# Kernel tuning notes

Hardware: AMD Instinct MI355X
Metric: run time of the kernel (lower is better)

Reference implementation:

```python
import jax, jax.numpy as jnp
import numpy as np

N_NODES = 100      # fixed: actor_fc expects 6000 = 100 * 60
IN_C    = 65536    # chev_conv_state_dim
OUT_C   = 60
K       = 3        # Chebyshev order
ACTION  = 100
N_EDGES = 1600


def setup_inputs() -> dict:
    key = jax.random.key(0)
    ks = jax.random.split(key, 20)
    s = 0.02  # small init scale
    f32 = jnp.float32
    return {
        "substrate_features": jax.random.normal(ks[0], (N_NODES, IN_C), f32),
        "substrate_edge_index": jax.random.randint(ks[1], (2, N_EDGES), 0, N_NODES),
        "vnr_features": jax.random.uniform(ks[2], (1, 3), f32),
        # ChebConv params: weight [K, IN_C, OUT_C], bias [OUT_C]
        "actor_cheb_w": (jax.random.normal(ks[3], (K, IN_C, OUT_C), f32) * s),
        "actor_cheb_b": jnp.zeros((OUT_C,), f32),
        "critic_cheb_w": (jax.random.normal(ks[4], (K, IN_C, OUT_C), f32) * s),
        "critic_cheb_b": jnp.zeros((OUT_C,), f32),
        # three Linear(1,60) per head, stacked: w [3, 60], b [3, 60]
        "actor_vnr_w": jax.random.normal(ks[5], (3, OUT_C), f32) * s,
        "actor_vnr_b": jnp.zeros((3, OUT_C), f32),
        "critic_vnr_w": jax.random.normal(ks[6], (3, OUT_C), f32) * s,
        "critic_vnr_b": jnp.zeros((3, OUT_C), f32),
        # heads
        "actor_fc_w": jax.random.normal(ks[7], (N_NODES * OUT_C, ACTION), f32) * s,
        "actor_fc_b": jnp.zeros((ACTION,), f32),
        "critic_fc_w": jax.random.normal(ks[8], (N_NODES * OUT_C, 1), f32) * s,
        "critic_fc_b": jnp.zeros((1,), f32),
    }


def _cheb_conv(x, src, dst, W, b):
    """PyG ChebConv with sym normalization, lambda_max=2 => L_hat = -D^-1/2 A D^-1/2.
    Z0 = x, Z1 = L_hat x, Z2 = 2 L_hat Z1 - Z0; out = sum_k Zk @ W[k] + b."""
    n = x.shape[0]
    ones = jnp.ones(src.shape[0], x.dtype)
    deg = jax.ops.segment_sum(ones, src, num_segments=n)
    dinv = jnp.where(deg > 0, jax.lax.rsqrt(jnp.maximum(deg, 1.0)), 0.0)
    w_norm = -dinv[src] * dinv[dst]  # [E]

    def lhat(z):  # sparse propagate: gather src rows, scale, scatter-add at dst
        return jax.ops.segment_sum(w_norm[:, None] * z[src], dst, num_segments=n)

    z0 = x
    z1 = lhat(z0)
    z2 = 2.0 * lhat(z1) - z0
    return z0 @ W[0] + z1 @ W[1] + z2 @ W[2] + b


def _vnr_sum(v, w, b):
    # sum of three Linear(1,60) outputs on scalars v[0], v[1], v[2] -> [60]
    return (v[:, None] * w + b).sum(axis=0)


def reference(substrate_features, substrate_edge_index, vnr_features,
              actor_cheb_w, actor_cheb_b, critic_cheb_w, critic_cheb_b,
              actor_vnr_w, actor_vnr_b, critic_vnr_w, critic_vnr_b,
              actor_fc_w, actor_fc_b, critic_fc_w, critic_fc_b):
    src, dst = substrate_edge_index[0], substrate_edge_index[1]
    v = vnr_features[0]  # [3]

    emb_a = jnp.tanh(_cheb_conv(substrate_features, src, dst, actor_cheb_w, actor_cheb_b))
    emb_a = emb_a + _vnr_sum(v, actor_vnr_w, actor_vnr_b)  # broadcast [N,60] + [60]
    flat_a = emb_a.reshape(1, -1)  # [1, 6000]
    logits = flat_a @ actor_fc_w + actor_fc_b  # [1, ACTION]

    emb_c = jnp.tanh(_cheb_conv(substrate_features, src, dst, critic_cheb_w, critic_cheb_b))
    emb_c = emb_c + _vnr_sum(v, critic_vnr_w, critic_vnr_b)
    flat_c = emb_c.reshape(1, -1)
    values = flat_c @ critic_fc_w + critic_fc_b  # [1, 1]

    return logits, values
```

## Files before the change

kernel.cpp:

```cpp
#include <hip/hip_runtime.h>
#include <math.h>

#define KDIM    65536
#define NNODES  100
#define OUTC    60
#define YW      64
#define YSLAB   (NNODES*YW)

#define BK5     64
#define ITERS5  16
#define SLAB5   (BK5*ITERS5)
#define NKC5    (KDIM/SLAB5)
#define CHUNK   256
#define NKC     256
#define STEPS   (CHUNK/32)

#define WS_S    0
#define WS_Y    10048
#define WS_E    48448
#define XB_OFF_BYTES   245760ull
#define XB_BYTES       (100ull*65536ull*2ull)
#define WS_NEED_BYTES  (XB_OFF_BYTES + XB_BYTES)
#define YP_OFF_BYTES   WS_NEED_BYTES
#define YP_FLOATS      ((size_t)NKC5 * 6 * YSLAB)
#define WS_NEED2_BYTES (YP_OFF_BYTES + YP_FLOATS * 4ull)

typedef short bf16x8 __attribute__((ext_vector_type(8)));
typedef float f32x4  __attribute__((ext_vector_type(4)));
typedef unsigned short ushort8 __attribute__((ext_vector_type(8)));

__device__ inline unsigned short f2bf(float f) {
    union { float f; unsigned u; } x; x.f = f;
    unsigned r = x.u + 0x7FFFu + ((x.u >> 16) & 1u);
    return (unsigned short)(r >> 16);
}

__global__ __launch_bounds__(256) void k_cvt_x(const float* __restrict__ x,
                                               ushort8* __restrict__ xb) {
    int g = blockIdx.x * 256 + threadIdx.x;
    for (int i = g; i < 819200; i += 204800) {
        const float4 lo = ((const float4*)x)[2 * i];
        const float4 hi = ((const float4*)x)[2 * i + 1];
        ushort8 o;
        o[0] = f2bf(lo.x); o[1] = f2bf(lo.y); o[2] = f2bf(lo.z); o[3] = f2bf(lo.w);
        o[4] = f2bf(hi.x); o[5] = f2bf(hi.y); o[6] = f2bf(hi.z); o[7] = f2bf(hi.w);
        xb[i] = o;
    }
}

template <bool DIRECT>
__global__ __launch_bounds__(512) void k_gemm6(const unsigned short* __restrict__ xb,
                                               const float* __restrict__ wa,
                                               const float* __restrict__ wc,
                                               float* __restrict__ Y,
                                               float* __restrict__ Yp) {
    __shared__ unsigned short Ab[2][112 * BK5];
    __shared__ float          Wf[2][4096];
    __shared__ float          padlds[256];
    const int hk   = blockIdx.x;
    const int kc   = blockIdx.y;
    const int wave = threadIdx.x >> 6;
    const int lane = threadIdx.x & 63;
    const int n16  = lane & 15;
    const int quad = lane >> 4;
    const int ng   = wave & 3;
    const int mg   = wave >> 2;
    const int c0   = ng * 16;
    const int cidx = min(c0 + n16, OUTC - 1);
    const int NT   = 4 - mg;
    const int kb0  = kc * SLAB5;

    const float* Wg = (hk < 3 ? wa : wc) + (size_t)(hk % 3) * ((size_t)KDIM * OUTC);

    auto DMA = [&](int buf, int kb) {
        const float* wsrc = Wg + (size_t)kb * OUTC;
#pragma unroll
        for (int j5 = 0; j5 < 4; ++j5) {
            int j = wave + j5 * 8;
            const void* src; void* dst;
            if (j < 16) {
                int chunk = j * 64 + lane;
                int m  = chunk >> 3;
                int cc = (chunk & 7) ^ (m & 7);
                src = xb + (size_t)min(m, NNODES - 1) * KDIM + kb + cc * 8;
                dst = (j < 14) ? (void*)&Ab[buf][j * 512] : (void*)padlds;
            } else {
                int jj = j - 16;
                src = wsrc + (jj == 15 ? 0 : jj * 256) + lane * 4;
                dst = &Wf[buf][jj * 256];
            }
            __builtin_amdgcn_global_load_lds(
                (const __attribute__((address_space(1))) void*)src,
                (__attribute__((address_space(3))) void*)dst, 16, 0, 0);
        }
    };

    DMA(0, kb0);
    f32x4 acc[4] = {};

#pragma unroll
    for (int it = 0; it < ITERS5; ++it) {
        if (it + 1 < ITERS5) {
            DMA((it + 1) & 1, kb0 + (it + 1) * BK5);
            asm volatile("s_waitcnt vmcnt(4)" ::: "memory");
        } else {
            asm volatile("s_waitcnt vmcnt(0)" ::: "memory");
        }
        __builtin_amdgcn_s_barrier();
        asm volatile("" ::: "memory");
        const unsigned short* A = Ab[it & 1];
        const float*          B = Wf[it & 1];
#pragma unroll
        for (int s = 0; s < 2; ++s) {
            bf16x8 bfr;
#pragma unroll
            for (int jq = 0; jq < 8; ++jq) {
                int jj = (jq + quad * 2) & 7;
                bfr[jj] = (short)f2bf(B[(s * 32 + quad * 8 + jj) * OUTC + cidx]);
            }
            int ch = (s * 4 + quad) ^ (n16 & 7);
#pragma unroll
            for (int t = 0; t < 4; ++t) {
                if (t < NT) {
                    int T = mg * 4 + t;
                    bf16x8 afr = *(const bf16x8*)(A + (T * 16 + n16) * BK5 + ch * 8);
                    acc[t] = __builtin_amdgcn_mfma_f32_16x16x32_bf16(afr, bfr, acc[t], 0, 0, 0);
                }
            }
        }
        asm volatile("" ::: "memory");
        __builtin_amdgcn_s_barrier();
    }

    float* Yb = DIRECT ? (Yp + ((size_t)kc * 6 + hk) * YSLAB) : (Y + hk * YSLAB);
#pragma unroll
    for (int t = 0; t < 4; ++t) {
        if (t < NT) {
            int T = mg * 4 + t;
#pragma unroll
            for (int r = 0; r < 4; ++r) {
                int row = T * 16 + quad * 4 + r;
                if (row < NNODES) {
                    if (DIRECT) Yb[row * YW + c0 + n16] = acc[t][r];
                    else        atomicAdd(&Yb[row * YW + c0 + n16], acc[t][r]);
                }
            }
        }
    }
}

__global__ __launch_bounds__(256) void k_reduce(const float* __restrict__ P,
                                                float* __restrict__ Y) {
    int g = blockIdx.x * 256 + threadIdx.x;
    if (g >= 9600) return;
    const f32x4* p = (const f32x4*)P + g;
    f32x4 s = {};
#pragma unroll 4
    for (int kc = 0; kc < NKC5; ++kc) s += p[(size_t)kc * 9600];
    ((f32x4*)Y)[g] = s;
}

__global__ __launch_bounds__(256, 2) void k_gemm_f32(const float* __restrict__ x,
                                                     const float* __restrict__ wa,
                                                     const float* __restrict__ wc,
                                                     float* __restrict__ Y) {
    const int hk   = blockIdx.x;
    const int kc   = blockIdx.y;
    const int wave = threadIdx.x >> 6;
    const int lane = threadIdx.x & 63;
    const int n16  = lane & 15;
    const int quad = lane >> 4;
    const float* W = (hk < 3 ? wa : wc) + (size_t)(hk % 3) * ((size_t)KDIM * OUTC);
    const int c0   = wave * 16;
    const int cidx = min(c0 + n16, OUTC - 1);
    const int kb0  = kc * CHUNK + quad * 8;
    const float* ap[7];
#pragma unroll
    for (int t = 0; t < 7; ++t)
        ap[t] = x + (size_t)min(n16 + 16 * t, NNODES - 1) * KDIM + kb0;
    const float* bp = W + (size_t)kb0 * OUTC + cidx;
    f32x4 acc[7] = {};
#pragma unroll 2
    for (int s = 0; s < STEPS; ++s) {
        bf16x8 bfr;
        const float* q = bp + (size_t)s * 32 * OUTC;
#pragma unroll
        for (int j = 0; j < 8; ++j) bfr[j] = (short)f2bf(q[j * OUTC]);
#pragma unroll
        for (int t = 0; t < 7; ++t) {
            const float* p = ap[t] + s * 32;
            float4 lo = *(const float4*)p;
            float4 hi = *(const float4*)(p + 4);
            bf16x8 afr;
            afr[0] = (short)f2bf(lo.x); afr[1] = (short)f2bf(lo.y);
            afr[2] = (short)f2bf(lo.z); afr[3] = (short)f2bf(lo.w);
            afr[4] = (short)f2bf(hi.x); afr[5] = (short)f2bf(hi.y);
            afr[6] = (short)f2bf(hi.z); afr[7] = (short)f2bf(hi.w);
            acc[t] = __builtin_amdgcn_mfma_f32_16x16x32_bf16(afr, bfr, acc[t], 0, 0, 0);
        }
    }
    float* Yb = Y + hk * YSLAB;
#pragma unroll
    for (int t = 0; t < 7; ++t)
#pragma unroll
        for (int r = 0; r < 4; ++r) {
            int row = t * 16 + quad * 4 + r;
            if (row < NNODES)
                atomicAdd(&Yb[row * YW + c0 + n16], acc[t][r]);
        }
}

__global__ __launch_bounds__(128) void k_emb(const int* __restrict__ ei,
                                             const float* __restrict__ Y,
                                             const float* __restrict__ vnr,
                                             const float* __restrict__ avw,
                                             const float* __restrict__ avb,
                                             const float* __restrict__ cvw,
                                             const float* __restrict__ cvb,
                                             const float* __restrict__ acb,
                                             const float* __restrict__ ccb,
                                             const float* __restrict__ afcb,
                                             const float* __restrict__ cfcb,
                                             float* __restrict__ E,
                                             float* __restrict__ out) {
    __shared__ float Sp[NNODES * 101];
    __shared__ float y0[NNODES], y1[NNODES], y2[NNODES], t2[NNODES];
    __shared__ int   deg[NNODES];
    __shared__ float dinv[NNODES];
    const int b = blockIdx.x, head = b / OUTC, c = b % OUTC;
    const int t = threadIdx.x;
    const int* src = ei;
    const int* dst = ei + 1600;

    for (int i = t; i < NNODES * 101; i += 128) Sp[i] = 0.f;
    if (t < NNODES) deg[t] = 0;
    __syncthreads();
    for (int e = t; e < 1600; e += 128) atomicAdd(&deg[src[e]], 1);
    __syncthreads();
    if (t < NNODES) { int d = deg[t]; dinv[t] = (d > 0) ? rsqrtf((float)d) : 0.f; }
    __syncthreads();
    for (int e = t; e < 1600; e += 128) {
        int s = src[e], d = dst[e];
        atomicAdd(&Sp[d * 101 + s], -dinv[s] * dinv[d]);
    }
    const float* Yh = Y + (size_t)head * 3 * YSLAB;
    if (t < NNODES) {
        y0[t] = Yh[t * YW + c];
        y1[t] = Yh[YSLAB + t * YW + c];
        y2[t] = Yh[2 * YSLAB + t * YW + c];
    }
    if (b == 0 && t < 101) out[t] = (t < 100) ? afcb[t] : cfcb[0];
    __syncthreads();

    float z1 = 0.f, s2 = 0.f;
    if (t < NNODES) {
        const float* sr = Sp + t * 101;
        for (int m = 0; m < NNODES; ++m) { z1 += sr[m] * y1[m]; s2 += sr[m] * y2[m]; }
        t2[t] = s2;
    }
    __syncthreads();
    if (t < NNODES) {
        const float* sr = Sp + t * 101;
        float t3 = 0.f;
        for (int m = 0; m < NNODES; ++m) t3 += sr[m] * t2[m];
        const float* cb = head ? ccb : acb;
        const float* vw = head ? cvw : avw;
        const float* vb = head ? cvb : avb;
        float u  = y0[t] + z1 + 2.f * t3 - y2[t] + cb[c];
        float vs = vnr[0] * vw[c]        + vb[c]
                 + vnr[1] * vw[OUTC + c] + vb[OUTC + c]
                 + vnr[2] * vw[2*OUTC+c] + vb[2*OUTC+c];
        E[head * (NNODES * OUTC) + t * OUTC + c] = tanhf(u) + vs;
    }
}

__global__ __launch_bounds__(128) void k_heads(const float* __restrict__ E,
                                               const float* __restrict__ afw,
                                               const float* __restrict__ cfw,
                                               float* __restrict__ out) {
    __shared__ float ea[25], ec[25];
    const int b = blockIdx.x, t = threadIdx.x;
    const int f0 = b * 25;
    if (t < 25) {
        ea[t] = E[f0 + t];
        ec[t] = E[NNODES * OUTC + f0 + t];
    }
    __syncthreads();
    if (t < 100) {
        float s = 0.f;
#pragma unroll
        for (int i = 0; i < 25; ++i) s += ea[i] * afw[(size_t)(f0 + i) * 100 + t];
        atomicAdd(&out[t], s);
    } else if (t == 100) {
        float s = 0.f;
#pragma unroll
        for (int i = 0; i < 25; ++i) s += ec[i] * cfw[f0 + i];
        atomicAdd(&out[100], s);
    }
}

extern "C" void kernel_launch(void* const* d_in, const int* in_sizes, int n_in,
                              void* d_out, int out_size, void* d_ws, size_t ws_size,
                              hipStream_t stream) {
    const float* x    = (const float*)d_in[0];
    const int*   ei   = (const int*)  d_in[1];
    const float* vnr  = (const float*)d_in[2];
    const float* wa   = (const float*)d_in[3];
    const float* acb  = (const float*)d_in[4];
    const float* wc   = (const float*)d_in[5];
    const float* ccb  = (const float*)d_in[6];
    const float* avw  = (const float*)d_in[7];
    const float* avb  = (const float*)d_in[8];
    const float* cvw  = (const float*)d_in[9];
    const float* cvb  = (const float*)d_in[10];
    const float* afw  = (const float*)d_in[11];
    const float* afcb = (const float*)d_in[12];
    const float* cfw  = (const float*)d_in[13];
    const float* cfcb = (const float*)d_in[14];

    float* ws = (float*)d_ws;
    float* Y  = ws + WS_Y;
    float* E  = ws + WS_E;
    float* out = (float*)d_out;

    if (ws_size >= WS_NEED2_BYTES) {
        unsigned short* xb = (unsigned short*)((char*)d_ws + XB_OFF_BYTES);
        float* Yp = (float*)((char*)d_ws + YP_OFF_BYTES);
        k_cvt_x<<<800, 256, 0, stream>>>(x, (ushort8*)xb);
        k_gemm6<true><<<dim3(6, NKC5), 512, 0, stream>>>(xb, wa, wc, Y, Yp);
        k_reduce<<<38, 256, 0, stream>>>(Yp, Y);
    } else if (ws_size >= WS_NEED_BYTES) {
        unsigned short* xb = (unsigned short*)((char*)d_ws + XB_OFF_BYTES);
        hipMemsetAsync((char*)d_ws + WS_Y * 4, 0, (WS_E - WS_Y) * 4, stream);
        k_cvt_x<<<800, 256, 0, stream>>>(x, (ushort8*)xb);
        k_gemm6<false><<<dim3(6, NKC5), 512, 0, stream>>>(xb, wa, wc, Y, nullptr);
    } else {
        hipMemsetAsync((char*)d_ws + WS_Y * 4, 0, (WS_E - WS_Y) * 4, stream);
        k_gemm_f32<<<dim3(6, NKC), 256, 0, stream>>>(x, wa, wc, Y);
    }

    k_emb<<<120, 128, 0, stream>>>(ei, Y, vnr, avw, avb, cvw, cvb,
                                   acb, ccb, afcb, cfcb, E, out);
    k_heads<<<240, 128, 0, stream>>>(E, afw, cfw, out);
}
```

Before: 237.4 us.

## Replace partial-sum GEMM with 256-thread kernel using register-prefetched weights and atomics

The bf16 GEMM is rewritten as k_gemm7: 256-thread blocks in which each wave covers all 7 row tiles of one 16-column slice. The weight operand is prefetched straight into registers, double-buffered, instead of being staged through LDS. The grid is flattened to 384 blocks with a remapped index order, and partial results are accumulated with atomics into Y, which k_cvt_x now zeroes. This removes the large partial buffer, the reduce kernel and the LDS traffic for weights. In exchange it adds atomic contention and uncoalesced strided global loads of the weights.

```diff
diff --git a/kernel.cpp b/kernel.cpp
--- a/kernel.cpp
+++ b/kernel.cpp
@@ -15,15 +15,11 @@
 #define NKC     256
 #define STEPS   (CHUNK/32)
 
-#define WS_S    0
 #define WS_Y    10048
 #define WS_E    48448
 #define XB_OFF_BYTES   245760ull
 #define XB_BYTES       (100ull*65536ull*2ull)
 #define WS_NEED_BYTES  (XB_OFF_BYTES + XB_BYTES)
-#define YP_OFF_BYTES   WS_NEED_BYTES
-#define YP_FLOATS      ((size_t)NKC5 * 6 * YSLAB)
-#define WS_NEED2_BYTES (YP_OFF_BYTES + YP_FLOATS * 4ull)
 
 typedef short bf16x8 __attribute__((ext_vector_type(8)));
 typedef float f32x4  __attribute__((ext_vector_type(4)));
@@ -36,8 +32,10 @@
 }
 
 __global__ __launch_bounds__(256) void k_cvt_x(const float* __restrict__ x,
-                                               ushort8* __restrict__ xb) {
+                                               ushort8* __restrict__ xb,
+                                               float* __restrict__ Y) {
     int g = blockIdx.x * 256 + threadIdx.x;
+    if (g < 9600) ((f32x4*)Y)[g] = (f32x4){};
     for (int i = g; i < 819200; i += 204800) {
         const float4 lo = ((const float4*)x)[2 * i];
         const float4 hi = ((const float4*)x)[2 * i + 1];
@@ -48,116 +46,92 @@
     }
 }
 
-template <bool DIRECT>
-__global__ __launch_bounds__(512) void k_gemm6(const unsigned short* __restrict__ xb,
+__global__ __launch_bounds__(256) void k_gemm7(const unsigned short* __restrict__ xb,
                                                const float* __restrict__ wa,
                                                const float* __restrict__ wc,
-                                               float* __restrict__ Y,
-                                               float* __restrict__ Yp) {
-    __shared__ unsigned short Ab[2][112 * BK5];
-    __shared__ float          Wf[2][4096];
-    __shared__ float          padlds[256];
-    const int hk   = blockIdx.x;
-    const int kc   = blockIdx.y;
+                                               float* __restrict__ Y) {
+    __shared__ unsigned short Ab[2][14 * 512];
+    __shared__ unsigned short padlds[512];
+    const int b    = blockIdx.x;
+    const int lo8  = b & 7, q = b >> 3;
+    const int hk   = q % 6;
+    const int kc   = lo8 + 8 * (q / 6);
     const int wave = threadIdx.x >> 6;
     const int lane = threadIdx.x & 63;
     const int n16  = lane & 15;
     const int quad = lane >> 4;
-    const int ng   = wave & 3;
-    const int mg   = wave >> 2;
-    const int c0   = ng * 16;
+    const int c0   = wave * 16;
     const int cidx = min(c0 + n16, OUTC - 1);
-    const int NT   = 4 - mg;
     const int kb0  = kc * SLAB5;
 
     const float* Wg = (hk < 3 ? wa : wc) + (size_t)(hk % 3) * ((size_t)KDIM * OUTC);
 
     auto DMA = [&](int buf, int kb) {
-        const float* wsrc = Wg + (size_t)kb * OUTC;
 #pragma unroll
         for (int j5 = 0; j5 < 4; ++j5) {
-            int j = wave + j5 * 8;
-            const void* src; void* dst;
-            if (j < 16) {
-                int chunk = j * 64 + lane;
-                int m  = chunk >> 3;
-                int cc = (chunk & 7) ^ (m & 7);
-                src = xb + (size_t)min(m, NNODES - 1) * KDIM + kb + cc * 8;
-                dst = (j < 14) ? (void*)&Ab[buf][j * 512] : (void*)padlds;
-            } else {
-                int jj = j - 16;
-                src = wsrc + (jj == 15 ? 0 : jj * 256) + lane * 4;
-                dst = &Wf[buf][jj * 256];
-            }
+            int j = wave + j5 * 4;
+            int chunk = j * 64 + lane;
+            int m  = chunk >> 3;
+            int cc = (chunk & 7) ^ (m & 7);
+            const unsigned short* src =
+                xb + (size_t)min(m, NNODES - 1) * KDIM + kb + cc * 8;
+            void* dst = (j < 14) ? (void*)&Ab[buf][j * 512] : (void*)padlds;
             __builtin_amdgcn_global_load_lds(
                 (const __attribute__((address_space(1))) void*)src,
                 (__attribute__((address_space(3))) void*)dst, 16, 0, 0);
         }
     };
 
+    float breg[2][16];
+    auto LOADB = [&](int pb, int kb) {
+        const float* base = Wg + (size_t)(kb + quad * 8) * OUTC + cidx;
+#pragma unroll
+        for (int s = 0; s < 2; ++s)
+#pragma unroll
+            for (int j = 0; j < 8; ++j)
+                breg[pb][s * 8 + j] = base[(s * 32 + j) * OUTC];
+    };
+
     DMA(0, kb0);
-    f32x4 acc[4] = {};
+    LOADB(0, kb0);
+    f32x4 acc[7] = {};
 
 #pragma unroll
     for (int it = 0; it < ITERS5; ++it) {
         if (it + 1 < ITERS5) {
             DMA((it + 1) & 1, kb0 + (it + 1) * BK5);
-            asm volatile("s_waitcnt vmcnt(4)" ::: "memory");
+            LOADB((it + 1) & 1, kb0 + (it + 1) * BK5);
+            asm volatile("s_waitcnt vmcnt(20)" ::: "memory");
         } else {
             asm volatile("s_waitcnt vmcnt(0)" ::: "memory");
         }
         __builtin_amdgcn_s_barrier();
-        asm volatile("" ::: "memory");
         const unsigned short* A = Ab[it & 1];
-        const float*          B = Wf[it & 1];
 #pragma unroll
         for (int s = 0; s < 2; ++s) {
             bf16x8 bfr;
 #pragma unroll
-            for (int jq = 0; jq < 8; ++jq) {
-                int jj = (jq + quad * 2) & 7;
-                bfr[jj] = (short)f2bf(B[(s * 32 + quad * 8 + jj) * OUTC + cidx]);
+            for (int j = 0; j < 8; ++j)
+                bfr[j] = (short)f2bf(breg[it & 1][s * 8 + j]);
+            int ch = (s * 4 + quad) ^ (n16 & 7);
+#pragma unroll
+            for (int t = 0; t < 7; ++t) {
+                bf16x8 afr = *(const bf16x8*)(A + (t * 16 + n16) * BK5 + ch * 8);
+                acc[t] = __builtin_amdgcn_mfma_f32_16x16x32_bf16(afr, bfr, acc[t], 0, 0, 0);
             }
-            int ch = (s * 4 + quad) ^ (n16 & 7);
-#pragma unroll
-            for (int t = 0; t < 4; ++t) {
-                if (t < NT) {
-                    int T = mg * 4 + t;
-                    bf16x8 afr = *(const bf16x8*)(A + (T * 16 + n16) * BK5 + ch * 8);
-                    acc[t] = __builtin_amdgcn_mfma_f32_16x16x32_bf16(afr, bfr, acc[t], 0, 0, 0);
-                }
-            }
-        }
-        asm volatile("" ::: "memory");
+        }
         __builtin_amdgcn_s_barrier();
     }
 
-    float* Yb = DIRECT ? (Yp + ((size_t)kc * 6 + hk) * YSLAB) : (Y + hk * YSLAB);
-#pragma unroll
-    for (int t = 0; t < 4; ++t) {
-        if (t < NT) {
-            int T = mg * 4 + t;
-#pragma unroll
-            for (int r = 0; r < 4; ++r) {
-                int row = T * 16 + quad * 4 + r;
-                if (row < NNODES) {
-                    if (DIRECT) Yb[row * YW + c0 + n16] = acc[t][r];
-                    else        atomicAdd(&Yb[row * YW + c0 + n16], acc[t][r]);
-                }
-            }
-        }
-    }
-}
-
-__global__ __launch_bounds__(256) void k_reduce(const float* __restrict__ P,
-                                                float* __restrict__ Y) {
-    int g = blockIdx.x * 256 + threadIdx.x;
-    if (g >= 9600) return;
-    const f32x4* p = (const f32x4*)P + g;
-    f32x4 s = {};
-#pragma unroll 4
-    for (int kc = 0; kc < NKC5; ++kc) s += p[(size_t)kc * 9600];
-    ((f32x4*)Y)[g] = s;
+    float* Yb = Y + hk * YSLAB;
+#pragma unroll
+    for (int t = 0; t < 7; ++t)
+#pragma unroll
+        for (int r = 0; r < 4; ++r) {
+            int row = t * 16 + quad * 4 + r;
+            if (row < NNODES)
+                atomicAdd(&Yb[row * YW + c0 + n16], acc[t][r]);
+        }
 }
 
 __global__ __launch_bounds__(256, 2) void k_gemm_f32(const float* __restrict__ x,
@@ -183,9 +157,9 @@
 #pragma unroll 2
     for (int s = 0; s < STEPS; ++s) {
         bf16x8 bfr;
-        const float* q = bp + (size_t)s * 32 * OUTC;
-#pragma unroll
-        for (int j = 0; j < 8; ++j) bfr[j] = (short)f2bf(q[j * OUTC]);
+        const float* qq = bp + (size_t)s * 32 * OUTC;
+#pragma unroll
+        for (int j = 0; j < 8; ++j) bfr[j] = (short)f2bf(qq[j * OUTC]);
 #pragma unroll
         for (int t = 0; t < 7; ++t) {
             const float* p = ap[t] + s * 32;
@@ -323,17 +297,10 @@
     float* E  = ws + WS_E;
     float* out = (float*)d_out;
 
-    if (ws_size >= WS_NEED2_BYTES) {
+    if (ws_size >= WS_NEED_BYTES) {
         unsigned short* xb = (unsigned short*)((char*)d_ws + XB_OFF_BYTES);
-        float* Yp = (float*)((char*)d_ws + YP_OFF_BYTES);
-        k_cvt_x<<<800, 256, 0, stream>>>(x, (ushort8*)xb);
-        k_gemm6<true><<<dim3(6, NKC5), 512, 0, stream>>>(xb, wa, wc, Y, Yp);
-        k_reduce<<<38, 256, 0, stream>>>(Yp, Y);
-    } else if (ws_size >= WS_NEED_BYTES) {
-        unsigned short* xb = (unsigned short*)((char*)d_ws + XB_OFF_BYTES);
-        hipMemsetAsync((char*)d_ws + WS_Y * 4, 0, (WS_E - WS_Y) * 4, stream);
-        k_cvt_x<<<800, 256, 0, stream>>>(x, (ushort8*)xb);
-        k_gemm6<false><<<dim3(6, NKC5), 512, 0, stream>>>(xb, wa, wc, Y, nullptr);
+        k_cvt_x<<<800, 256, 0, stream>>>(x, (ushort8*)xb, Y);
+        k_gemm7<<<384, 256, 0, stream>>>(xb, wa, wc, Y);
     } else {
         hipMemsetAsync((char*)d_ws + WS_Y * 4, 0, (WS_E - WS_Y) * 4, stream);
         k_gemm_f32<<<dim3(6, NKC), 256, 0, stream>>>(x, wa, wc, Y);
```

New measurement: 204.4 us. 1.16x faster.
